# Performance work log

Measured on AMD Instinct MI355X. Metric: run time of the kernel, lower is better.

## Reference

```python
import jax, jax.numpy as jnp
import numpy as np

T, B, H, L, V = 256, 64, 1024, 2, 32000
Hh = H // 2
MAX_FORGET = 0.875  # forget gate z in (1-max_forget, 1)


def setup_inputs() -> dict:
    key = jax.random.key(0)
    ks = jax.random.split(key, 12)
    s = 0.02
    def w(k, shape):
        return (jax.random.normal(k, shape, jnp.float32) * s)
    return {
        "input_seq": jax.random.randint(ks[0], (T, B), 0, V),
        "h0": jax.random.normal(ks[1], (L, B, H), jnp.float32),
        "emb": w(ks[2], (V, H)),
        "W_zr1": w(ks[3], (L, H + Hh, H)),   "b_zr1": jnp.zeros((L, H), jnp.float32),
        "W_g1":  w(ks[4], (L, H + Hh, Hh)), "b_g1":  jnp.zeros((L, Hh), jnp.float32),
        "W_zr2": w(ks[5], (L, H + Hh, H)),   "b_zr2": jnp.zeros((L, H), jnp.float32),
        "W_g2":  w(ks[6], (L, H + Hh, Hh)), "b_g2":  jnp.zeros((L, Hh), jnp.float32),
    }


def _revgru_cell(x, h, Wzr1, bzr1, Wg1, bg1, Wzr2, bzr2, Wg2, bg2):
    # x: [B,H], h: [B,H] split into two halves that update each other (reversible GRU)
    h1, h2 = h[:, :Hh], h[:, Hh:]
    zr1 = jnp.concatenate([x, h2], axis=1) @ Wzr1 + bzr1
    z1 = jax.nn.sigmoid(zr1[:, :Hh]) * MAX_FORGET + (1.0 - MAX_FORGET)
    r1 = jax.nn.sigmoid(zr1[:, Hh:])
    g1 = jnp.tanh(jnp.concatenate([x, r1 * h2], axis=1) @ Wg1 + bg1)
    h1n = z1 * h1 + (1.0 - z1) * g1
    zr2 = jnp.concatenate([x, h1n], axis=1) @ Wzr2 + bzr2
    z2 = jax.nn.sigmoid(zr2[:, :Hh]) * MAX_FORGET + (1.0 - MAX_FORGET)
    r2 = jax.nn.sigmoid(zr2[:, Hh:])
    g2 = jnp.tanh(jnp.concatenate([x, r2 * h1n], axis=1) @ Wg2 + bg2)
    h2n = z2 * h2 + (1.0 - z2) * g2
    return jnp.concatenate([h1n, h2n], axis=1)


def reference(input_seq, h0, emb, W_zr1, b_zr1, W_g1, b_g1, W_zr2, b_zr2, W_g2, b_g2):
    # Dropout rates are 0 (module defaults), so all locked-dropout layers are identity.
    x_seq = emb[input_seq]  # [T,B,H]

    def step(hiddens, x_t):  # hiddens: [L,B,H]
        cur = x_t
        new = []
        for l in range(L):
            hn = _revgru_cell(cur, hiddens[l], W_zr1[l], b_zr1[l], W_g1[l], b_g1[l],
                              W_zr2[l], b_zr2[l], W_g2[l], b_g2[l])
            new.append(hn)
            cur = hn  # output_hidden feeds next layer (lockdroph is identity)
        return jnp.stack(new), None

    final, _ = jax.lax.scan(step, h0, x_seq)
    return final  # [L,B,H] last hidden per layer
```

## Files before the change

kernel.cpp:

```cpp
#include <hip/hip_runtime.h>

#define T_   256
#define B_   64
#define H_   1024
#define Hh_  512
#define L_   2
#define K1_  1536
#define MAXF 0.875f
#define NBLK 128
#define NT   1024

#define OFF_WZR1 0u
#define OFF_WG1  3145728u
#define OFF_WZR2 4718592u
#define OFF_WG2  7864320u
#define OFF_XT   9437184u
#define OFF_HT   9568256u
#define OFF_ZT   9830400u
#define OFF_RHT  9895936u
#define OFF_CTR  9961472u

__global__ __launch_bounds__(256) void retile_w(const float* __restrict__ src,
                                                float* __restrict__ dst,
                                                int N, int C) {
    size_t tid = (size_t)blockIdx.x * 256 + threadIdx.x;
    size_t total = (size_t)L_ * K1_ * N;
    if (tid >= total) return;
    int c = (int)(tid % C);
    int k = (int)((tid / C) % K1_);
    int b = (int)((tid / ((size_t)C * K1_)) % (N / C));
    int l = (int)(tid / ((size_t)C * K1_ * (N / C)));
    dst[tid] = src[((size_t)l * K1_ + k) * N + b * C + c];
}

__device__ __forceinline__ float ld_coh(const float* p) {
    return __hip_atomic_load(p, __ATOMIC_RELAXED, __HIP_MEMORY_SCOPE_AGENT);
}
__device__ __forceinline__ void st_coh(float* p, float v) {
    __hip_atomic_store(p, v, __ATOMIC_RELAXED, __HIP_MEMORY_SCOPE_AGENT);
}

__device__ __forceinline__ void gbar(unsigned* ctr, unsigned* target) {
    *target += NBLK;
    __syncthreads();
    if (threadIdx.x == 0) {
        __hip_atomic_fetch_add(ctr, 1u, __ATOMIC_RELAXED, __HIP_MEMORY_SCOPE_AGENT);
        while (__hip_atomic_load(ctr, __ATOMIC_RELAXED, __HIP_MEMORY_SCOPE_AGENT) < *target)
            __builtin_amdgcn_s_sleep(1);
    }
    __syncthreads();
}

template<int C>
__device__ __forceinline__ float phase_gemm(const float* __restrict__ Axlo,
                                            const float* __restrict__ Ahi,
                                            const float* __restrict__ Wt,
                                            float* __restrict__ red) {
    const int tid  = threadIdx.x;
    const int lane = tid & 63;
    const int w    = __builtin_amdgcn_readfirstlane(tid >> 6);
    const int k0   = w * 96;
    for (int i = tid; i < 64 * (C + 1); i += NT) red[i] = 0.f;
    float acc[C];
#pragma unroll
    for (int c = 0; c < C; ++c) acc[c] = 0.f;
    __syncthreads();
#pragma unroll 1
    for (int kb = 0; kb < 96; kb += 8) {
        float av[8];
#pragma unroll
        for (int j = 0; j < 8; ++j) {
            const int k = k0 + kb + j;
            const float* ap = (k < H_) ? (Axlo + (size_t)k * 64)
                                       : (Ahi + (size_t)(k - H_) * 64);
            av[j] = ld_coh(ap + lane);
        }
#pragma unroll
        for (int j = 0; j < 8; ++j) {
            const float* wr = Wt + (size_t)(k0 + kb + j) * C;
#pragma unroll
            for (int c = 0; c < C; ++c) acc[c] = fmaf(av[j], wr[c], acc[c]);
        }
    }
#pragma unroll
    for (int c = 0; c < C; ++c) atomicAdd(&red[lane * (C + 1) + c], acc[c]);
    __syncthreads();
    float v = 0.f;
    if (tid < 64 * C) v = red[(tid / C) * (C + 1) + (tid % C)];
    return v;
}

__global__ __launch_bounds__(NT) void revgru_main(
    const int* __restrict__ seq, const float* __restrict__ h0,
    const float* __restrict__ emb,
    const float* __restrict__ bzr1, const float* __restrict__ bg1,
    const float* __restrict__ bzr2, const float* __restrict__ bg2,
    float* __restrict__ ws, float* __restrict__ out)
{
    const int bi = blockIdx.x, tid = threadIdx.x;
    const int l = (bi >= 64) ? 1 : 0, bl = bi & 63;
    __shared__ float red[64 * 17];
    unsigned target = 0;

    float* xT  = ws + OFF_XT;
    float* hT  = ws + OFF_HT;
    float* zT  = ws + OFF_ZT;
    float* rhT = ws + OFF_RHT;
    unsigned* ctr = (unsigned*)(ws + OFF_CTR);

    const float* Wz1  = ws + OFF_WZR1 + ((size_t)l * 64 + bl) * K1_ * 16;
    const float* Wg1l = ws + OFF_WG1  + ((size_t)l * 64 + bl) * K1_ * 8;
    const float* Wz2  = ws + OFF_WZR2 + ((size_t)l * 64 + bl) * K1_ * 16;
    const float* Wg2l = ws + OFF_WG2  + ((size_t)l * 64 + bl) * K1_ * 8;

    const int gtid = bi * NT + tid;
    {
        int ll = gtid >> 16, rem = gtid & 65535, r = rem >> 10, n = rem & 1023;
        st_coh(&hT[(((size_t)ll * 2 + 1) * H_ + n) * 64 + r], h0[gtid]);
        if (bi < 64) {
            int k = gtid >> 6, rr = gtid & 63;
            st_coh(&xT[gtid], emb[(size_t)seq[rr] * H_ + k]);
        }
    }
    gbar(ctr, &target);

    for (int s = 0; s <= T_; ++s) {
        const int t = (l == 0) ? s : s - 1;
        const bool act = (t >= 0) && (t < T_);
        const int buf = t & 1;
        float* hC = hT + ((size_t)l * 2 + buf) * (H_ * 64);
        float* hP = hT + ((size_t)l * 2 + (buf ^ 1)) * (H_ * 64);
        const float* Ax = (l == 0) ? (xT + (size_t)buf * (H_ * 64))
                                   : (hT + (size_t)buf * (H_ * 64));
        float* zl  = zT  + (size_t)l * Hh_ * 64;
        float* rhl = rhT + (size_t)l * Hh_ * 64;

        if (act) {
            float v = phase_gemm<16>(Ax, hP + Hh_ * 64, Wz1, red);
            int r = tid >> 4, c = tid & 15, n = bl * 16 + c;
            v += bzr1[l * H_ + n];
            float sg = 1.f / (1.f + __expf(-v));
            if (n < Hh_) st_coh(&zl[n * 64 + r], sg * MAXF + (1.f - MAXF));
            else st_coh(&rhl[(n - Hh_) * 64 + r],
                        sg * ld_coh(&hP[(size_t)n * 64 + r]));
            if (l == 0 && t + 1 < T_) {
                int k = gtid >> 6, rr = gtid & 63;
                st_coh(&xT[(size_t)((t + 1) & 1) * (H_ * 64) + k * 64 + rr],
                       emb[(size_t)seq[(t + 1) * B_ + rr] * H_ + k]);
            }
        }
        gbar(ctr, &target);
        if (act) {
            float v = phase_gemm<8>(Ax, rhl, Wg1l, red);
            if (tid < 512) {
                int r = tid >> 3, c = tid & 7, n = bl * 8 + c;
                float g = tanhf(v + bg1[l * Hh_ + n]);
                float z = ld_coh(&zl[n * 64 + r]);
                float h1o = ld_coh(&hP[(size_t)n * 64 + r]);
                st_coh(&hC[(size_t)n * 64 + r], z * h1o + (1.f - z) * g);
            }
        }
        gbar(ctr, &target);
        if (act) {
            float v = phase_gemm<16>(Ax, hC, Wz2, red);
            int r = tid >> 4, c = tid & 15, n = bl * 16 + c;
            v += bzr2[l * H_ + n];
            float sg = 1.f / (1.f + __expf(-v));
            if (n < Hh_) st_coh(&zl[n * 64 + r], sg * MAXF + (1.f - MAXF));
            else st_coh(&rhl[(n - Hh_) * 64 + r],
                        sg * ld_coh(&hC[(size_t)(n - Hh_) * 64 + r]));
        }
        gbar(ctr, &target);
        if (act) {
            float v = phase_gemm<8>(Ax, rhl, Wg2l, red);
            if (tid < 512) {
                int r = tid >> 3, c = tid & 7, n = bl * 8 + c;
                float g = tanhf(v + bg2[l * Hh_ + n]);
                float z = ld_coh(&zl[n * 64 + r]);
                float h2o = ld_coh(&hP[(size_t)(Hh_ + n) * 64 + r]);
                st_coh(&hC[(size_t)(Hh_ + n) * 64 + r], z * h2o + (1.f - z) * g);
            }
        }
        gbar(ctr, &target);
    }
    {
        int ll = gtid >> 16, rem = gtid & 65535, r = rem >> 10, n = rem & 1023;
        out[gtid] = ld_coh(&hT[(((size_t)ll * 2 + 1) * H_ + n) * 64 + r]);
    }
}

extern "C" void kernel_launch(void* const* d_in, const int* in_sizes, int n_in,
                              void* d_out, int out_size, void* d_ws, size_t ws_size,
                              hipStream_t stream) {
    (void)in_sizes; (void)n_in; (void)out_size; (void)ws_size;
    const int*   seq  = (const int*)  d_in[0];
    const float* h0   = (const float*)d_in[1];
    const float* emb  = (const float*)d_in[2];
    const float* Wzr1 = (const float*)d_in[3];
    const float* bzr1 = (const float*)d_in[4];
    const float* Wg1  = (const float*)d_in[5];
    const float* bg1  = (const float*)d_in[6];
    const float* Wzr2 = (const float*)d_in[7];
    const float* bzr2 = (const float*)d_in[8];
    const float* Wg2  = (const float*)d_in[9];
    const float* bg2  = (const float*)d_in[10];
    float* out = (float*)d_out;
    float* ws  = (float*)d_ws;

    hipMemsetAsync((char*)d_ws + (size_t)OFF_CTR * 4, 0, 64, stream);
    retile_w<<<12288, 256, 0, stream>>>(Wzr1, ws + OFF_WZR1, H_, 16);
    retile_w<<<6144,  256, 0, stream>>>(Wg1,  ws + OFF_WG1,  Hh_, 8);
    retile_w<<<12288, 256, 0, stream>>>(Wzr2, ws + OFF_WZR2, H_, 16);
    retile_w<<<6144,  256, 0, stream>>>(Wg2,  ws + OFF_WG2,  Hh_, 8);

    void* args[] = { &seq, &h0, &emb, &bzr1, &bg1, &bzr2, &bg2, &ws, &out };
    hipLaunchCooperativeKernel((void*)revgru_main, dim3(NBLK), dim3(NT),
                               args, 0, stream);
}
```

Before: 48.10 ms.

## Stage activation panels into per-XCD scratch copies with XCD-local barriers

Each block reads its XCC id and takes a rank within its (XCD, layer) group. Before each GEMM phase, the blocks in that group cooperatively copy the needed activation rows into a scratch buffer owned by the XCD, then meet at an XCD-local barrier. The GEMM then reads the scratch buffer with sc0 loads (inline asm) that can hit the XCD-local L2, where before it read shared coherent data with uncached atomic loads. This adds one extra barrier and one extra copy per phase. In phases that reuse the x rows, those rows are restaged even though they did not change.

Measured after the change: 58.03 ms. 20.6% more time.

```diff
diff --git a/kernel.cpp b/kernel.cpp
--- a/kernel.cpp
+++ b/kernel.cpp
@@ -19,6 +19,9 @@
 #define OFF_ZT   9830400u
 #define OFF_RHT  9895936u
 #define OFF_CTR  9961472u
+#define OFF_GCNT 9961504u
+#define OFF_XBAR 9961536u
+#define OFF_SCR  9961600u
 
 __global__ __launch_bounds__(256) void retile_w(const float* __restrict__ src,
                                                 float* __restrict__ dst,
@@ -40,6 +43,12 @@
     __hip_atomic_store(p, v, __ATOMIC_RELAXED, __HIP_MEMORY_SCOPE_AGENT);
 }
 
+__device__ __forceinline__ int xcc_id() {
+    int x;
+    asm volatile("s_getreg_b32 %0, hwreg(HW_REG_XCC_ID)" : "=s"(x));
+    return x & 7;
+}
+
 __device__ __forceinline__ void gbar(unsigned* ctr, unsigned* target) {
     *target += NBLK;
     __syncthreads();
@@ -51,9 +60,35 @@
     __syncthreads();
 }
 
+__device__ __forceinline__ void xgbar(unsigned* xctr, unsigned* xtarget, int gcount) {
+    *xtarget += (unsigned)gcount;
+    __syncthreads();
+    if (threadIdx.x == 0) {
+        __hip_atomic_fetch_add(xctr, 1u, __ATOMIC_RELAXED, __HIP_MEMORY_SCOPE_AGENT);
+        while (__hip_atomic_load(xctr, __ATOMIC_RELAXED, __HIP_MEMORY_SCOPE_AGENT) < *xtarget)
+            __builtin_amdgcn_s_sleep(1);
+    }
+    __syncthreads();
+}
+
+__device__ __forceinline__ void stage_panel(const float* __restrict__ lo,
+                                            const float* __restrict__ hi,
+                                            float* __restrict__ scr,
+                                            int rank, int gcount, bool full) {
+    const int kb   = full ? 0 : H_;
+    const int rows = K1_ - kb;
+    const int k0   = kb + rank * rows / gcount;
+    const int k1   = kb + (rank + 1) * rows / gcount;
+    for (int i = k0 * 64 + (int)threadIdx.x; i < k1 * 64; i += NT) {
+        const int k = i >> 6;
+        const float* sp = (k < H_) ? (lo + (size_t)k * 64)
+                                   : (hi + (size_t)(k - H_) * 64);
+        scr[i] = ld_coh(sp + (i & 63));
+    }
+}
+
 template<int C>
-__device__ __forceinline__ float phase_gemm(const float* __restrict__ Axlo,
-                                            const float* __restrict__ Ahi,
+__device__ __forceinline__ float phase_gemm(const float* __restrict__ scr,
                                             const float* __restrict__ Wt,
                                             float* __restrict__ red) {
     const int tid  = threadIdx.x;
@@ -67,14 +102,24 @@
     __syncthreads();
 #pragma unroll 1
     for (int kb = 0; kb < 96; kb += 8) {
-        float av[8];
-#pragma unroll
-        for (int j = 0; j < 8; ++j) {
-            const int k = k0 + kb + j;
-            const float* ap = (k < H_) ? (Axlo + (size_t)k * 64)
-                                       : (Ahi + (size_t)(k - H_) * 64);
-            av[j] = ld_coh(ap + lane);
-        }
+        unsigned long long ap =
+            (unsigned long long)(scr + (size_t)(k0 + kb) * 64 + lane);
+        float a0, a1, a2, a3, a4, a5, a6, a7;
+        asm volatile(
+            "global_load_dword %0, %8, off sc0\n\t"
+            "global_load_dword %1, %8, off offset:256 sc0\n\t"
+            "global_load_dword %2, %8, off offset:512 sc0\n\t"
+            "global_load_dword %3, %8, off offset:768 sc0\n\t"
+            "global_load_dword %4, %8, off offset:1024 sc0\n\t"
+            "global_load_dword %5, %8, off offset:1280 sc0\n\t"
+            "global_load_dword %6, %8, off offset:1536 sc0\n\t"
+            "global_load_dword %7, %8, off offset:1792 sc0\n\t"
+            "s_waitcnt vmcnt(0)"
+            : "=v"(a0), "=v"(a1), "=v"(a2), "=v"(a3),
+              "=v"(a4), "=v"(a5), "=v"(a6), "=v"(a7)
+            : "v"(ap)
+            : "memory");
+        const float av[8] = {a0, a1, a2, a3, a4, a5, a6, a7};
 #pragma unroll
         for (int j = 0; j < 8; ++j) {
             const float* wr = Wt + (size_t)(k0 + kb + j) * C;
@@ -100,18 +145,32 @@
     const int bi = blockIdx.x, tid = threadIdx.x;
     const int l = (bi >= 64) ? 1 : 0, bl = bi & 63;
     __shared__ float red[64 * 17];
-    unsigned target = 0;
+    __shared__ int s_xcd, s_rank, s_gcnt;
+    unsigned target = 0, xtarget = 0;
 
     float* xT  = ws + OFF_XT;
     float* hT  = ws + OFF_HT;
     float* zT  = ws + OFF_ZT;
     float* rhT = ws + OFF_RHT;
-    unsigned* ctr = (unsigned*)(ws + OFF_CTR);
+    unsigned* ctr  = (unsigned*)(ws + OFF_CTR);
+    unsigned* gcnt = (unsigned*)(ws + OFF_GCNT);
+    unsigned* xbar = (unsigned*)(ws + OFF_XBAR);
 
     const float* Wz1  = ws + OFF_WZR1 + ((size_t)l * 64 + bl) * K1_ * 16;
     const float* Wg1l = ws + OFF_WG1  + ((size_t)l * 64 + bl) * K1_ * 8;
     const float* Wz2  = ws + OFF_WZR2 + ((size_t)l * 64 + bl) * K1_ * 16;
     const float* Wg2l = ws + OFF_WG2  + ((size_t)l * 64 + bl) * K1_ * 8;
+
+    if (tid == 0) {
+        int x = xcc_id();
+        s_xcd = x;
+        s_rank = (int)__hip_atomic_fetch_add(&gcnt[x * 2 + l], 1u,
+                     __ATOMIC_RELAXED, __HIP_MEMORY_SCOPE_AGENT);
+    }
+    __syncthreads();
+    const int xcd = s_xcd, rank = s_rank;
+    float* scr = ws + OFF_SCR + ((size_t)xcd * 2 + l) * ((size_t)K1_ * 64);
+    unsigned* xctr = &xbar[xcd * 2 + l];
 
     const int gtid = bi * NT + tid;
     {
@@ -123,6 +182,11 @@
         }
     }
     gbar(ctr, &target);
+    if (tid == 0)
+        s_gcnt = (int)__hip_atomic_load(&gcnt[xcd * 2 + l],
+                     __ATOMIC_RELAXED, __HIP_MEMORY_SCOPE_AGENT);
+    __syncthreads();
+    const int gcount = s_gcnt;
 
     for (int s = 0; s <= T_; ++s) {
         const int t = (l == 0) ? s : s - 1;
@@ -135,8 +199,10 @@
         float* zl  = zT  + (size_t)l * Hh_ * 64;
         float* rhl = rhT + (size_t)l * Hh_ * 64;
 
-        if (act) {
-            float v = phase_gemm<16>(Ax, hP + Hh_ * 64, Wz1, red);
+        if (act) stage_panel(Ax, hP + Hh_ * 64, scr, rank, gcount, true);
+        xgbar(xctr, &xtarget, gcount);
+        if (act) {
+            float v = phase_gemm<16>(scr, Wz1, red);
             int r = tid >> 4, c = tid & 15, n = bl * 16 + c;
             v += bzr1[l * H_ + n];
             float sg = 1.f / (1.f + __expf(-v));
@@ -150,8 +216,10 @@
             }
         }
         gbar(ctr, &target);
-        if (act) {
-            float v = phase_gemm<8>(Ax, rhl, Wg1l, red);
+        if (act) stage_panel(Ax, rhl, scr, rank, gcount, false);
+        xgbar(xctr, &xtarget, gcount);
+        if (act) {
+            float v = phase_gemm<8>(scr, Wg1l, red);
             if (tid < 512) {
                 int r = tid >> 3, c = tid & 7, n = bl * 8 + c;
                 float g = tanhf(v + bg1[l * Hh_ + n]);
@@ -161,8 +229,10 @@
             }
         }
         gbar(ctr, &target);
-        if (act) {
-            float v = phase_gemm<16>(Ax, hC, Wz2, red);
+        if (act) stage_panel(Ax, hC, scr, rank, gcount, false);
+        xgbar(xctr, &xtarget, gcount);
+        if (act) {
+            float v = phase_gemm<16>(scr, Wz2, red);
             int r = tid >> 4, c = tid & 15, n = bl * 16 + c;
             v += bzr2[l * H_ + n];
             float sg = 1.f / (1.f + __expf(-v));
@@ -171,8 +241,10 @@
                         sg * ld_coh(&hC[(size_t)(n - Hh_) * 64 + r]));
         }
         gbar(ctr, &target);
-        if (act) {
-            float v = phase_gemm<8>(Ax, rhl, Wg2l, red);
+        if (act) stage_panel(Ax, rhl, scr, rank, gcount, false);
+        xgbar(xctr, &xtarget, gcount);
+        if (act) {
+            float v = phase_gemm<8>(scr, Wg2l, red);
             if (tid < 512) {
                 int r = tid >> 3, c = tid & 7, n = bl * 8 + c;
                 float g = tanhf(v + bg2[l * Hh_ + n]);
@@ -207,7 +279,7 @@
     float* out = (float*)d_out;
     float* ws  = (float*)d_ws;
 
-    hipMemsetAsync((char*)d_ws + (size_t)OFF_CTR * 4, 0, 64, stream);
+    hipMemsetAsync((char*)d_ws + (size_t)OFF_CTR * 4, 0, 512, stream);
     retile_w<<<12288, 256, 0, stream>>>(Wzr1, ws + OFF_WZR1, H_, 16);
     retile_w<<<6144,  256, 0, stream>>>(Wg1,  ws + OFF_WG1,  Hh_, 8);
     retile_w<<<12288, 256, 0, stream>>>(Wzr2, ws + OFF_WZR2, H_, 16);
```

## Split input projections onto helper blocks and pipeline them ahead of recurrent chain

Applied to the files above, without the earlier changes.

Doubles the grid to 256 blocks. The extra 128 helper blocks compute the input-side (x) contributions of all four gate GEMMs one step ahead and write them to a workspace buffer. The 128 chain blocks then only do the recurrent 512-wide K portion and use per-layer hierarchical barriers inside each time step, with one global barrier per step. This shortens the serial critical path and replaces the single global counter barrier with grouped counters polled by a wavefront. In exchange it adds extra workspace traffic, needs all 256 1024-thread blocks to be co-resident, and uses a three-stage skew with a parity-indexed buffer that must stay race-free.

Result: faster. 46.99 ms (-2.3%).

```diff
diff --git a/kernel.cpp b/kernel.cpp
--- a/kernel.cpp
+++ b/kernel.cpp
@@ -7,7 +7,7 @@
 #define L_   2
 #define K1_  1536
 #define MAXF 0.875f
-#define NBLK 128
+#define NBLK 256
 #define NT   1024
 
 #define OFF_WZR1 0u
@@ -18,7 +18,8 @@
 #define OFF_HT   9568256u
 #define OFF_ZT   9830400u
 #define OFF_RHT  9895936u
-#define OFF_CTR  9961472u
+#define OFF_XC   9961472u
+#define OFF_BARS 10747904u
 
 __global__ __launch_bounds__(256) void retile_w(const float* __restrict__ src,
                                                 float* __restrict__ dst,
@@ -40,47 +41,48 @@
     __hip_atomic_store(p, v, __ATOMIC_RELAXED, __HIP_MEMORY_SCOPE_AGENT);
 }
 
-__device__ __forceinline__ void gbar(unsigned* ctr, unsigned* target) {
-    *target += NBLK;
-    __syncthreads();
-    if (threadIdx.x == 0) {
-        __hip_atomic_fetch_add(ctr, 1u, __ATOMIC_RELAXED, __HIP_MEMORY_SCOPE_AGENT);
-        while (__hip_atomic_load(ctr, __ATOMIC_RELAXED, __HIP_MEMORY_SCOPE_AGENT) < *target)
+__device__ __forceinline__ void tbar(unsigned* ctrs, int ncnt, int group,
+                                     unsigned* round) {
+    *round += 1;
+    const unsigned need = 4u * *round;
+    __syncthreads();
+    if (threadIdx.x < 64) {
+        if (threadIdx.x == 0)
+            __hip_atomic_fetch_add(&ctrs[group], 1u, __ATOMIC_RELAXED,
+                                   __HIP_MEMORY_SCOPE_AGENT);
+        const int j = (int)threadIdx.x & (ncnt - 1);
+        for (;;) {
+            unsigned v = __hip_atomic_load(&ctrs[j], __ATOMIC_RELAXED,
+                                           __HIP_MEMORY_SCOPE_AGENT);
+            if (__all(v >= need)) break;
             __builtin_amdgcn_s_sleep(1);
+        }
     }
     __syncthreads();
 }
 
 template<int C>
-__device__ __forceinline__ float phase_gemm(const float* __restrict__ Axlo,
-                                            const float* __restrict__ Ahi,
-                                            const float* __restrict__ Wt,
-                                            float* __restrict__ red) {
+__device__ __forceinline__ float dep_gemm(const float* __restrict__ Apanel,
+                                          const float* __restrict__ Wt,
+                                          float* __restrict__ red) {
     const int tid  = threadIdx.x;
     const int lane = tid & 63;
     const int w    = __builtin_amdgcn_readfirstlane(tid >> 6);
-    const int k0   = w * 96;
+    const int k0   = w * 32;
     for (int i = tid; i < 64 * (C + 1); i += NT) red[i] = 0.f;
+    float av[32];
+#pragma unroll
+    for (int j = 0; j < 32; ++j)
+        av[j] = ld_coh(Apanel + (size_t)(k0 + j) * 64 + lane);
     float acc[C];
 #pragma unroll
     for (int c = 0; c < C; ++c) acc[c] = 0.f;
     __syncthreads();
-#pragma unroll 1
-    for (int kb = 0; kb < 96; kb += 8) {
-        float av[8];
-#pragma unroll
-        for (int j = 0; j < 8; ++j) {
-            const int k = k0 + kb + j;
-            const float* ap = (k < H_) ? (Axlo + (size_t)k * 64)
-                                       : (Ahi + (size_t)(k - H_) * 64);
-            av[j] = ld_coh(ap + lane);
-        }
-#pragma unroll
-        for (int j = 0; j < 8; ++j) {
-            const float* wr = Wt + (size_t)(k0 + kb + j) * C;
-#pragma unroll
-            for (int c = 0; c < C; ++c) acc[c] = fmaf(av[j], wr[c], acc[c]);
-        }
+#pragma unroll
+    for (int j = 0; j < 32; ++j) {
+        const float* wr = Wt + (size_t)(H_ + k0 + j) * C;
+#pragma unroll
+        for (int c = 0; c < C; ++c) acc[c] = fmaf(av[j], wr[c], acc[c]);
     }
 #pragma unroll
     for (int c = 0; c < C; ++c) atomicAdd(&red[lane * (C + 1) + c], acc[c]);
@@ -88,6 +90,54 @@
     float v = 0.f;
     if (tid < 64 * C) v = red[(tid / C) * (C + 1) + (tid % C)];
     return v;
+}
+
+__device__ __forceinline__ void helper_gemm(const float* __restrict__ Apanel,
+                                            const float* __restrict__ Wz1t,
+                                            const float* __restrict__ Wg1t,
+                                            const float* __restrict__ Wz2t,
+                                            const float* __restrict__ Wg2t,
+                                            float* __restrict__ red,
+                                            float* __restrict__ XcOut) {
+    const int tid  = threadIdx.x;
+    const int lane = tid & 63;
+    const int w    = __builtin_amdgcn_readfirstlane(tid >> 6);
+    const int k0   = w * 64;
+    for (int i = tid; i < 64 * 49; i += NT) red[i] = 0.f;
+    float acc[48];
+#pragma unroll
+    for (int c = 0; c < 48; ++c) acc[c] = 0.f;
+    __syncthreads();
+#pragma unroll 1
+    for (int kb = 0; kb < 64; kb += 8) {
+        float av[8];
+#pragma unroll
+        for (int j = 0; j < 8; ++j)
+            av[j] = ld_coh(Apanel + (size_t)(k0 + kb + j) * 64 + lane);
+#pragma unroll
+        for (int j = 0; j < 8; ++j) {
+            const int k = k0 + kb + j;
+            const float* w1 = Wz1t + (size_t)k * 16;
+            const float* g1 = Wg1t + (size_t)k * 8;
+            const float* w2 = Wz2t + (size_t)k * 16;
+            const float* g2 = Wg2t + (size_t)k * 8;
+#pragma unroll
+            for (int c = 0; c < 16; ++c) acc[c]      = fmaf(av[j], w1[c], acc[c]);
+#pragma unroll
+            for (int c = 0; c < 8;  ++c) acc[16 + c] = fmaf(av[j], g1[c], acc[16 + c]);
+#pragma unroll
+            for (int c = 0; c < 16; ++c) acc[24 + c] = fmaf(av[j], w2[c], acc[24 + c]);
+#pragma unroll
+            for (int c = 0; c < 8;  ++c) acc[40 + c] = fmaf(av[j], g2[c], acc[40 + c]);
+        }
+    }
+#pragma unroll
+    for (int c = 0; c < 48; ++c) atomicAdd(&red[lane * 49 + c], acc[c]);
+    __syncthreads();
+    for (int i = tid; i < 48 * 64; i += NT) {
+        int cs = i >> 6, r = i & 63;
+        st_coh(&XcOut[(size_t)cs * 64 + r], red[r * 49 + cs]);
+    }
 }
 
 __global__ __launch_bounds__(NT) void revgru_main(
@@ -98,94 +148,118 @@
     float* __restrict__ ws, float* __restrict__ out)
 {
     const int bi = blockIdx.x, tid = threadIdx.x;
-    const int l = (bi >= 64) ? 1 : 0, bl = bi & 63;
-    __shared__ float red[64 * 17];
-    unsigned target = 0;
+    const bool isChain = (bi < 128);
+    const int l  = isChain ? (bi >> 6) : ((bi - 128) >> 6);
+    const int bl = bi & 63;
+    __shared__ float red[64 * 49];
+    unsigned rG = 0, rC = 0;
 
     float* xT  = ws + OFF_XT;
     float* hT  = ws + OFF_HT;
     float* zT  = ws + OFF_ZT;
     float* rhT = ws + OFF_RHT;
-    unsigned* ctr = (unsigned*)(ws + OFF_CTR);
+    unsigned* barC0 = (unsigned*)(ws + OFF_BARS);
+    unsigned* barC1 = barC0 + 16;
+    unsigned* barG  = barC0 + 32;
 
     const float* Wz1  = ws + OFF_WZR1 + ((size_t)l * 64 + bl) * K1_ * 16;
     const float* Wg1l = ws + OFF_WG1  + ((size_t)l * 64 + bl) * K1_ * 8;
     const float* Wz2  = ws + OFF_WZR2 + ((size_t)l * 64 + bl) * K1_ * 16;
     const float* Wg2l = ws + OFF_WG2  + ((size_t)l * 64 + bl) * K1_ * 8;
 
-    const int gtid = bi * NT + tid;
-    {
+    if (bi < 128) {
+        int gtid = bi * NT + tid;
         int ll = gtid >> 16, rem = gtid & 65535, r = rem >> 10, n = rem & 1023;
         st_coh(&hT[(((size_t)ll * 2 + 1) * H_ + n) * 64 + r], h0[gtid]);
-        if (bi < 64) {
-            int k = gtid >> 6, rr = gtid & 63;
-            st_coh(&xT[gtid], emb[(size_t)seq[rr] * H_ + k]);
-        }
-    }
-    gbar(ctr, &target);
-
-    for (int s = 0; s <= T_; ++s) {
-        const int t = (l == 0) ? s : s - 1;
-        const bool act = (t >= 0) && (t < T_);
-        const int buf = t & 1;
-        float* hC = hT + ((size_t)l * 2 + buf) * (H_ * 64);
-        float* hP = hT + ((size_t)l * 2 + (buf ^ 1)) * (H_ * 64);
-        const float* Ax = (l == 0) ? (xT + (size_t)buf * (H_ * 64))
-                                   : (hT + (size_t)buf * (H_ * 64));
-        float* zl  = zT  + (size_t)l * Hh_ * 64;
-        float* rhl = rhT + (size_t)l * Hh_ * 64;
-
-        if (act) {
-            float v = phase_gemm<16>(Ax, hP + Hh_ * 64, Wz1, red);
-            int r = tid >> 4, c = tid & 15, n = bl * 16 + c;
-            v += bzr1[l * H_ + n];
-            float sg = 1.f / (1.f + __expf(-v));
-            if (n < Hh_) st_coh(&zl[n * 64 + r], sg * MAXF + (1.f - MAXF));
-            else st_coh(&rhl[(n - Hh_) * 64 + r],
-                        sg * ld_coh(&hP[(size_t)n * 64 + r]));
-            if (l == 0 && t + 1 < T_) {
-                int k = gtid >> 6, rr = gtid & 63;
-                st_coh(&xT[(size_t)((t + 1) & 1) * (H_ * 64) + k * 64 + rr],
-                       emb[(size_t)seq[(t + 1) * B_ + rr] * H_ + k]);
+    } else if (bi < 192) {
+        int g2i = (bi - 128) * NT + tid;
+        int k = g2i >> 6, rr = g2i & 63;
+        st_coh(&xT[(size_t)k * 64 + rr], emb[(size_t)seq[rr] * H_ + k]);
+    }
+    tbar(barG, 64, bi >> 2, &rG);
+
+    for (int s = 0; s <= 258; ++s) {
+        if (isChain) {
+            const int t = s - 1 - 2 * l;
+            if (t >= 0 && t < T_) {
+                const int par = t & 1;
+                float* hC = hT + ((size_t)l * 2 + par) * (H_ * 64);
+                float* hP = hT + ((size_t)l * 2 + (par ^ 1)) * (H_ * 64);
+                float* zl  = zT  + (size_t)l * Hh_ * 64;
+                float* rhl = rhT + (size_t)l * Hh_ * 64;
+                const float* Xcb = ws + OFF_XC +
+                    (((size_t)l * 2 + par) * 64 + bl) * (48 * 64);
+                unsigned* barC = l ? barC1 : barC0;
+
+                {
+                    int r = tid >> 4, c = tid & 15, n = bl * 16 + c;
+                    float xc = ld_coh(&Xcb[(size_t)c * 64 + r]) + bzr1[l * H_ + n];
+                    float hv = ld_coh(&hP[(size_t)n * 64 + r]);
+                    float v = dep_gemm<16>(hP + Hh_ * 64, Wz1, red) + xc;
+                    float sg = 1.f / (1.f + __expf(-v));
+                    if (n < Hh_) st_coh(&zl[n * 64 + r], sg * MAXF + (1.f - MAXF));
+                    else st_coh(&rhl[(n - Hh_) * 64 + r], sg * hv);
+                }
+                tbar(barC, 16, bl >> 2, &rC);
+                {
+                    int tt = tid & 511, r = tt >> 3, c = tt & 7, n = bl * 8 + c;
+                    float xc  = ld_coh(&Xcb[(size_t)(16 + c) * 64 + r]) + bg1[l * Hh_ + n];
+                    float z   = ld_coh(&zl[n * 64 + r]);
+                    float h1o = ld_coh(&hP[(size_t)n * 64 + r]);
+                    float v = dep_gemm<8>(rhl, Wg1l, red);
+                    if (tid < 512) {
+                        float g = tanhf(v + xc);
+                        st_coh(&hC[(size_t)n * 64 + r], z * h1o + (1.f - z) * g);
+                    }
+                }
+                tbar(barC, 16, bl >> 2, &rC);
+                {
+                    int r = tid >> 4, c = tid & 15, n = bl * 16 + c;
+                    float xc = ld_coh(&Xcb[(size_t)(24 + c) * 64 + r]) + bzr2[l * H_ + n];
+                    float hv = ld_coh(&hC[(size_t)((n >= Hh_) ? (n - Hh_) : n) * 64 + r]);
+                    float v = dep_gemm<16>(hC, Wz2, red) + xc;
+                    float sg = 1.f / (1.f + __expf(-v));
+                    if (n < Hh_) st_coh(&zl[n * 64 + r], sg * MAXF + (1.f - MAXF));
+                    else st_coh(&rhl[(n - Hh_) * 64 + r], sg * hv);
+                }
+                tbar(barC, 16, bl >> 2, &rC);
+                {
+                    int tt = tid & 511, r = tt >> 3, c = tt & 7, n = bl * 8 + c;
+                    float xc  = ld_coh(&Xcb[(size_t)(40 + c) * 64 + r]) + bg2[l * Hh_ + n];
+                    float z   = ld_coh(&zl[n * 64 + r]);
+                    float h2o = ld_coh(&hP[(size_t)(Hh_ + n) * 64 + r]);
+                    float v = dep_gemm<8>(rhl, Wg2l, red);
+                    if (tid < 512) {
+                        float g = tanhf(v + xc);
+                        st_coh(&hC[(size_t)(Hh_ + n) * 64 + r], z * h2o + (1.f - z) * g);
+                    }
+                }
             }
-        }
-        gbar(ctr, &target);
-        if (act) {
-            float v = phase_gemm<8>(Ax, rhl, Wg1l, red);
-            if (tid < 512) {
-                int r = tid >> 3, c = tid & 7, n = bl * 8 + c;
-                float g = tanhf(v + bg1[l * Hh_ + n]);
-                float z = ld_coh(&zl[n * 64 + r]);
-                float h1o = ld_coh(&hP[(size_t)n * 64 + r]);
-                st_coh(&hC[(size_t)n * 64 + r], z * h1o + (1.f - z) * g);
+        } else {
+            const int th = s - 2 * l;
+            if (th >= 0 && th < T_) {
+                const int par = th & 1;
+                const float* Ap = (l == 0) ? (xT + (size_t)par * (H_ * 64))
+                                           : (hT + (size_t)par * (H_ * 64));
+                float* XcOut = ws + OFF_XC +
+                    (((size_t)l * 2 + par) * 64 + bl) * (48 * 64);
+                helper_gemm(Ap, Wz1, Wg1l, Wz2, Wg2l, red, XcOut);
+                if (l == 0 && th + 1 < T_) {
+                    int g2i = bl * NT + tid;
+                    int k = g2i >> 6, rr = g2i & 63;
+                    st_coh(&xT[(size_t)((th + 1) & 1) * (H_ * 64) + (size_t)k * 64 + rr],
+                           emb[(size_t)seq[(th + 1) * B_ + rr] * H_ + k]);
+                }
             }
         }
-        gbar(ctr, &target);
-        if (act) {
-            float v = phase_gemm<16>(Ax, hC, Wz2, red);
-            int r = tid >> 4, c = tid & 15, n = bl * 16 + c;
-            v += bzr2[l * H_ + n];
-            float sg = 1.f / (1.f + __expf(-v));
-            if (n < Hh_) st_coh(&zl[n * 64 + r], sg * MAXF + (1.f - MAXF));
-            else st_coh(&rhl[(n - Hh_) * 64 + r],
-                        sg * ld_coh(&hC[(size_t)(n - Hh_) * 64 + r]));
-        }
-        gbar(ctr, &target);
-        if (act) {
-            float v = phase_gemm<8>(Ax, rhl, Wg2l, red);
-            if (tid < 512) {
-                int r = tid >> 3, c = tid & 7, n = bl * 8 + c;
-                float g = tanhf(v + bg2[l * Hh_ + n]);
-                float z = ld_coh(&zl[n * 64 + r]);
-                float h2o = ld_coh(&hP[(size_t)(Hh_ + n) * 64 + r]);
-                st_coh(&hC[(size_t)(Hh_ + n) * 64 + r], z * h2o + (1.f - z) * g);
-            }
-        }
-        gbar(ctr, &target);
+        tbar(barG, 64, bi >> 2, &rG);
     }
     {
-        int ll = gtid >> 16, rem = gtid & 65535, r = rem >> 10, n = rem & 1023;
-        out[gtid] = ld_coh(&hT[(((size_t)ll * 2 + 1) * H_ + n) * 64 + r]);
+        if (bi < 128) {
+            int gtid = bi * NT + tid;
+            int ll = gtid >> 16, rem = gtid & 65535, r = rem >> 10, n = rem & 1023;
+            out[gtid] = ld_coh(&hT[(((size_t)ll * 2 + 1) * H_ + n) * 64 + r]);
+        }
     }
 }
 
@@ -207,7 +281,7 @@
     float* out = (float*)d_out;
     float* ws  = (float*)d_ws;
 
-    hipMemsetAsync((char*)d_ws + (size_t)OFF_CTR * 4, 0, 64, stream);
+    hipMemsetAsync((char*)d_ws + (size_t)OFF_BARS * 4, 0, 512, stream);
     retile_w<<<12288, 256, 0, stream>>>(Wzr1, ws + OFF_WZR1, H_, 16);
     retile_w<<<6144,  256, 0, stream>>>(Wg1,  ws + OFF_WG1,  Hh_, 8);
     retile_w<<<12288, 256, 0, stream>>>(Wzr2, ws + OFF_WZR2, H_, 16);
```
